# Optimization experiments

Measured on AMD Instinct MI355X. Metric: run time of the kernel, lower is better.

Reference implementation:

```python
import jax, jax.numpy as jnp
import numpy as np

EMBED_DIM = 4096
NQ = 32           # query heads
NKV = 8           # kv heads
HEAD = 128        # head dim
KV_SEQ = 4096
B = 8
T = 32
START_POS = 4064  # end_pos = 4096
SCALE = 1.0 / np.sqrt(HEAD)
THETA = 10000.0


def _rope(x, table_len):
    """Faithful replication of the torch module's RoPE, including its bug:
    the torch code unpacks (B,H,T,D)=x.shape on a (B,T_seq,H,D) tensor, so the
    frequency table (of length table_len) is sliced to the first H (=num heads)
    rows and broadcast along the HEAD axis, not the sequence axis.
    x: (B, T_seq, H, D) float32.
    """
    Bn, Tn, H, D = x.shape
    dh = D // 2
    inv_freq = 1.0 / (THETA ** (jnp.arange(dh, dtype=jnp.float32) / dh))  # (dh,)
    pos = jnp.arange(table_len, dtype=jnp.float32)
    freqs = (pos[:, None] * inv_freq[None, :])[:H]  # (H, dh) -- head-indexed!
    cos = jnp.cos(freqs)[None, None]  # (1,1,H,dh)
    sin = jnp.sin(freqs)[None, None]
    xr, xi = x[..., 0::2], x[..., 1::2]  # complex pairs are consecutive elems
    yr = xr * cos - xi * sin
    yi = xr * sin + xi * cos
    return jnp.stack([yr, yi], axis=-1).reshape(Bn, Tn, H, D)


def setup_inputs() -> dict:
    key = jax.random.key(0)
    ks = jax.random.split(key, 5)
    x = jax.random.normal(ks[0], (B, T, EMBED_DIM), dtype=jnp.float32)
    Wq = jax.random.normal(ks[1], (EMBED_DIM, EMBED_DIM), dtype=jnp.float32) * 0.02
    Wk = jax.random.normal(ks[2], (NKV * HEAD, EMBED_DIM), dtype=jnp.float32) * 0.02
    Wv = jax.random.normal(ks[3], (NKV * HEAD, EMBED_DIM), dtype=jnp.float32) * 0.02
    Wo = jax.random.normal(ks[4], (EMBED_DIM, EMBED_DIM), dtype=jnp.float32) * 0.02
    cache_keys = jnp.zeros((B, KV_SEQ * 2, NKV, HEAD), dtype=jnp.float32)
    cache_values = jnp.zeros((B, KV_SEQ * 2, NKV, HEAD), dtype=jnp.float32)
    return {"x": x, "start_pos": START_POS, "cache_keys": cache_keys,
            "cache_values": cache_values, "Wq": Wq, "Wk": Wk, "Wv": Wv, "Wo": Wo}


def reference(x, start_pos, cache_keys, cache_values, Wq, Wk, Wv, Wo):
    Bn, Tn, C = x.shape
    q = (x @ Wq.T).reshape(Bn, Tn, NQ, HEAD)
    k = (x @ Wk.T).reshape(Bn, Tn, NKV, HEAD)
    v = (x @ Wv.T).reshape(Bn, Tn, NKV, HEAD)
    # rope=True branch: q table built for Tn positions, k table for KV_SEQ
    q = _rope(q, Tn)
    k = _rope(k, KV_SEQ)
    end = start_pos + Tn
    # cache write (torch detaches k/v before writing and reads detached views)
    ck = cache_keys.at[:Bn, start_pos:end].set(jax.lax.stop_gradient(k))
    cv = cache_values.at[:Bn, start_pos:end].set(jax.lax.stop_gradient(v))
    k_full = jax.lax.stop_gradient(ck[:Bn, :end])  # (B, end, NKV, D)
    v_full = jax.lax.stop_gradient(cv[:Bn, :end])
    r = NQ // NKV
    kf = jnp.repeat(k_full.transpose(0, 2, 1, 3), r, axis=1)  # (B, NQ, end, D)
    vf = jnp.repeat(v_full.transpose(0, 2, 1, 3), r, axis=1)
    qh = q.transpose(0, 2, 1, 3)                               # (B, NQ, T, D)
    att = jnp.einsum('bhtd,bhsd->bhts', qh, kf) * SCALE        # (B, NQ, T, end)
    causal = jnp.triu(jnp.ones((end, end), dtype=bool), 1)[-Tn:]  # (T, end)
    att = jnp.where(causal[None, None], -jnp.inf, att)
    att = jax.nn.softmax(att, axis=-1)
    out = jnp.einsum('bhts,bhsd->bhtd', att, vf)
    out = out.transpose(0, 2, 1, 3).reshape(Bn, Tn, C)
    return out @ Wo.T
```

## Files before the change

### kernel.cpp

```cpp
#include <hip/hip_runtime.h>
#include <stdint.h>

#define Bb 8
#define Tt 32
#define Ee 4096
#define NQ 32
#define NKV 8
#define HD 128
#define CACHE_S 8192
#define SSPLIT 8
#define SCALE_F 0.08838834764831845f

typedef _Float16 half8 __attribute__((ext_vector_type(8)));
typedef _Float16 half4 __attribute__((ext_vector_type(4)));
typedef float f32x4 __attribute__((ext_vector_type(4)));

static __device__ __forceinline__ _Float16 f2h(float f) { return (_Float16)f; }

__global__ __launch_bounds__(256) void gemm_nt(
    const float* __restrict__ A, const float* __restrict__ W,
    const float* __restrict__ W2, int n_split,
    float* __restrict__ C, int K, int ldc) {
  __shared__ _Float16 As[64][72];
  __shared__ _Float16 Ws[64][72];
  const int n0 = blockIdx.x * 64;
  const int m0 = blockIdx.y * 64;
  const float* Wp = (n0 < n_split) ? W : W2;
  const int nr0 = (n0 < n_split) ? n0 : (n0 - n_split);
  const int tid = threadIdx.x;
  const int lane = tid & 63;
  const int wave = tid >> 6;
  const int wm = (wave >> 1) * 32;
  const int wn = (wave & 1) * 32;
  const int l15 = lane & 15;
  const int quad = lane >> 4;
  const int sr = tid >> 4;
  const int sc = (tid & 15) * 4;

  f32x4 acc[2][2];
#pragma unroll
  for (int i = 0; i < 2; i++)
#pragma unroll
    for (int j = 0; j < 2; j++) acc[i][j] = f32x4{0.f, 0.f, 0.f, 0.f};

  float4 pa[4], pw[4];
#pragma unroll
  for (int p = 0; p < 4; p++) {
    const int r = sr + p * 16;
    pa[p] = *(const float4*)&A[(size_t)(m0 + r) * K + sc];
    pw[p] = *(const float4*)&Wp[(size_t)(nr0 + r) * K + sc];
  }

  for (int k0 = 0; k0 < K; k0 += 64) {
    __syncthreads();
#pragma unroll
    for (int p = 0; p < 4; p++) {
      const int r = sr + p * 16;
      half4 ha = {f2h(pa[p].x), f2h(pa[p].y), f2h(pa[p].z), f2h(pa[p].w)};
      *(half4*)&As[r][sc] = ha;
      half4 hw = {f2h(pw[p].x), f2h(pw[p].y), f2h(pw[p].z), f2h(pw[p].w)};
      *(half4*)&Ws[r][sc] = hw;
    }
    __syncthreads();
    if (k0 + 64 < K) {
#pragma unroll
      for (int p = 0; p < 4; p++) {
        const int r = sr + p * 16;
        pa[p] = *(const float4*)&A[(size_t)(m0 + r) * K + (k0 + 64 + sc)];
        pw[p] = *(const float4*)&Wp[(size_t)(nr0 + r) * K + (k0 + 64 + sc)];
      }
    }
#pragma unroll
    for (int ks = 0; ks < 2; ks++) {
      const int kc = ks * 32 + quad * 8;
      half8 af[2], wf[2];
#pragma unroll
      for (int i = 0; i < 2; i++) {
        af[i] = *(const half8*)&As[wm + i * 16 + l15][kc];
        wf[i] = *(const half8*)&Ws[wn + i * 16 + l15][kc];
      }
#pragma unroll
      for (int i = 0; i < 2; i++)
#pragma unroll
        for (int j = 0; j < 2; j++)
          acc[i][j] = __builtin_amdgcn_mfma_f32_16x16x32_f16(af[i], wf[j],
                                                             acc[i][j], 0, 0, 0);
    }
  }
#pragma unroll
  for (int i = 0; i < 2; i++) {
    const int mr = m0 + wm + i * 16 + quad * 4;
#pragma unroll
    for (int j = 0; j < 2; j++) {
      const int nc = n0 + wn + j * 16 + l15;
#pragma unroll
      for (int r = 0; r < 4; r++)
        C[(size_t)(mr + r) * ldc + nc] = acc[i][j][r];
    }
  }
}

__global__ __launch_bounds__(256) void rope_scatter(
    const float* __restrict__ qkv, float* __restrict__ qw,
    float* __restrict__ kw, float* __restrict__ vw) {
  const int pid = blockIdx.x * 256 + threadIdx.x;
  const int m = pid / 3072;
  const int c = pid - m * 3072;
  const int n = c * 2;
  const int b = m >> 5;
  const int t = m & 31;
  const float a0 = qkv[(size_t)m * 6144 + n];
  const float a1 = qkv[(size_t)m * 6144 + n + 1];
  if (n < 4096) {
    const int h = n >> 7;
    const int j = (n & 127) >> 1;
    const float invf = powf(10000.0f, -(float)j * (1.0f / 64.0f));
    float sn, cs;
    sincosf((float)h * invf, &sn, &cs);
    float* dst = qw + ((size_t)(b * NQ + h) * Tt + t) * HD + (j << 1);
    dst[0] = a0 * cs - a1 * sn;
    dst[1] = a0 * sn + a1 * cs;
  } else if (n < 5120) {
    const int nn = n - 4096;
    const int h = nn >> 7;
    const int j = (nn & 127) >> 1;
    const float invf = powf(10000.0f, -(float)j * (1.0f / 64.0f));
    float sn, cs;
    sincosf((float)h * invf, &sn, &cs);
    float* dst = kw + ((size_t)(b * NKV + h) * Tt + t) * HD + (j << 1);
    dst[0] = a0 * cs - a1 * sn;
    dst[1] = a0 * sn + a1 * cs;
  } else {
    const int nn = n - 5120;
    const int h = nn >> 7;
    const int d = nn & 127;
    float* dst = vw + ((size_t)(b * NKV + h) * Tt + t) * HD + d;
    dst[0] = a0;
    dst[1] = a1;
  }
}

__global__ __launch_bounds__(256) void attn_partial(
    const float* __restrict__ qw, const float* __restrict__ kw,
    const float* __restrict__ vw, const float* __restrict__ cacheK,
    const float* __restrict__ cacheV, const int* __restrict__ startp,
    float* __restrict__ pO, float* __restrict__ pM, float* __restrict__ pL) {
  const int blk = blockIdx.x;
  const int split = blk & (SSPLIT - 1);
  const int g = (blk / SSPLIT) & (NKV - 1);
  const int b = blk / (SSPLIT * NKV);
  const int start = *startp;
  const int end = start + Tt;
  int cl = ((end + SSPLIT * 32 - 1) / (SSPLIT * 32)) * 32;
  const int s_begin = split * cl;
  int s_end = s_begin + cl;
  if (s_end > end) s_end = end;

  const int tid = threadIdx.x;
  const int lane = tid & 63;
  const int wave = tid >> 6;
  const int l15 = lane & 15;
  const int quad = lane >> 4;
  const int h = g * 4 + wave;

  __shared__ _Float16 Ks[32][136];
  __shared__ _Float16 Vt[128][40];
  __shared__ _Float16 Ps[4][32][40];

  half8 qf[2][4];
#pragma unroll
  for (int mt = 0; mt < 2; mt++) {
    const int t = mt * 16 + l15;
    const float* qrow = qw + ((size_t)(b * NQ + h) * Tt + t) * HD;
#pragma unroll
    for (int ks = 0; ks < 4; ks++) {
      const int d0 = ks * 32 + quad * 8;
      float4 v0 = *(const float4*)&qrow[d0];
      float4 v1 = *(const float4*)&qrow[d0 + 4];
      half8 hq = {f2h(v0.x), f2h(v0.y), f2h(v0.z), f2h(v0.w),
                  f2h(v1.x), f2h(v1.y), f2h(v1.z), f2h(v1.w)};
      qf[mt][ks] = hq;
    }
  }

  f32x4 Oacc[2][8];
#pragma unroll
  for (int mt = 0; mt < 2; mt++)
#pragma unroll
    for (int dt = 0; dt < 8; dt++) Oacc[mt][dt] = f32x4{0.f, 0.f, 0.f, 0.f};
  float mrow[2][4], lrow[2][4];
#pragma unroll
  for (int mt = 0; mt < 2; mt++)
#pragma unroll
    for (int rr = 0; rr < 4; rr++) { mrow[mt][rr] = -1e30f; lrow[mt][rr] = 0.f; }

  const int str = tid >> 3;
  const int stc = (tid & 7) * 4;

  float4 pk[4], pv[4];
  auto load_chunk = [&](int s0) {
    const int sg = s0 + str;
    const bool valid = sg < end;
    const float* krow;
    const float* vrow;
    if (sg < start) {
      const size_t off = (((size_t)b * CACHE_S + sg) * NKV + g) * HD;
      krow = cacheK + off;
      vrow = cacheV + off;
    } else {
      int loc = sg - start;
      if (loc > Tt - 1) loc = Tt - 1;
      const size_t off = ((size_t)(b * NKV + g) * Tt + loc) * HD;
      krow = kw + off;
      vrow = vw + off;
    }
#pragma unroll
    for (int u = 0; u < 4; u++) {
      const int cc = stc + u * 32;
      pk[u] = valid ? *(const float4*)&krow[cc] : make_float4(0.f, 0.f, 0.f, 0.f);
      pv[u] = valid ? *(const float4*)&vrow[cc] : make_float4(0.f, 0.f, 0.f, 0.f);
    }
  };

  load_chunk(s_begin);

  for (int s0 = s_begin; s0 < s_end; s0 += 32) {
    __syncthreads();
#pragma unroll
    for (int u = 0; u < 4; u++) {
      const int cc = stc + u * 32;
      half4 hk = {f2h(pk[u].x), f2h(pk[u].y), f2h(pk[u].z), f2h(pk[u].w)};
      *(half4*)&Ks[str][cc] = hk;
      Vt[cc + 0][str] = f2h(pv[u].x);
      Vt[cc + 1][str] = f2h(pv[u].y);
      Vt[cc + 2][str] = f2h(pv[u].z);
      Vt[cc + 3][str] = f2h(pv[u].w);
    }
    __syncthreads();
    if (s0 + 32 < s_end) load_chunk(s0 + 32);

    f32x4 st[2][2];
#pragma unroll
    for (int mt = 0; mt < 2; mt++)
#pragma unroll
      for (int nt = 0; nt < 2; nt++) st[mt][nt] = f32x4{0.f, 0.f, 0.f, 0.f};
#pragma unroll
    for (int nt = 0; nt < 2; nt++) {
#pragma unroll
      for (int ks = 0; ks < 4; ks++) {
        half8 kf = *(const half8*)&Ks[nt * 16 + l15][ks * 32 + quad * 8];
        st[0][nt] = __builtin_amdgcn_mfma_f32_16x16x32_f16(qf[0][ks], kf, st[0][nt], 0, 0, 0);
        st[1][nt] = __builtin_amdgcn_mfma_f32_16x16x32_f16(qf[1][ks], kf, st[1][nt], 0, 0, 0);
      }
    }
#pragma unroll
    for (int mt = 0; mt < 2; mt++)
#pragma unroll
      for (int nt = 0; nt < 2; nt++)
#pragma unroll
        for (int rr = 0; rr < 4; rr++) {
          const int t = mt * 16 + quad * 4 + rr;
          const int sg = s0 + nt * 16 + l15;
          const float sv = st[mt][nt][rr] * SCALE_F;
          const bool masked = (sg > start + t) || (sg >= end);
          st[mt][nt][rr] = masked ? -1e30f : sv;
        }
#pragma unroll
    for (int mt = 0; mt < 2; mt++) {
      float rmax[4], rsum[4], al[4];
#pragma unroll
      for (int rr = 0; rr < 4; rr++)
        rmax[rr] = fmaxf(st[mt][0][rr], st[mt][1][rr]);
      for (int mm = 1; mm < 16; mm <<= 1)
#pragma unroll
        for (int rr = 0; rr < 4; rr++)
          rmax[rr] = fmaxf(rmax[rr], __shfl_xor(rmax[rr], mm));
#pragma unroll
      for (int rr = 0; rr < 4; rr++) {
        const float mn = fmaxf(mrow[mt][rr], rmax[rr]);
        al[rr] = __expf(mrow[mt][rr] - mn);
        mrow[mt][rr] = mn;
      }
#pragma unroll
      for (int nt = 0; nt < 2; nt++)
#pragma unroll
        for (int rr = 0; rr < 4; rr++)
          st[mt][nt][rr] = __expf(st[mt][nt][rr] - mrow[mt][rr]);
#pragma unroll
      for (int rr = 0; rr < 4; rr++) rsum[rr] = st[mt][0][rr] + st[mt][1][rr];
      for (int mm = 1; mm < 16; mm <<= 1)
#pragma unroll
        for (int rr = 0; rr < 4; rr++) rsum[rr] += __shfl_xor(rsum[rr], mm);
#pragma unroll
      for (int rr = 0; rr < 4; rr++)
        lrow[mt][rr] = lrow[mt][rr] * al[rr] + rsum[rr];
#pragma unroll
      for (int nt = 0; nt < 2; nt++)
#pragma unroll
        for (int rr = 0; rr < 4; rr++)
          Ps[wave][mt * 16 + quad * 4 + rr][nt * 16 + l15] = f2h(st[mt][nt][rr]);
#pragma unroll
      for (int dt = 0; dt < 8; dt++)
#pragma unroll
        for (int rr = 0; rr < 4; rr++) Oacc[mt][dt][rr] *= al[rr];
    }
    half8 pf0 = *(const half8*)&Ps[wave][l15][quad * 8];
    half8 pf1 = *(const half8*)&Ps[wave][16 + l15][quad * 8];
#pragma unroll
    for (int dt = 0; dt < 8; dt++) {
      half8 vf = *(const half8*)&Vt[dt * 16 + l15][quad * 8];
      Oacc[0][dt] = __builtin_amdgcn_mfma_f32_16x16x32_f16(pf0, vf, Oacc[0][dt], 0, 0, 0);
      Oacc[1][dt] = __builtin_amdgcn_mfma_f32_16x16x32_f16(pf1, vf, Oacc[1][dt], 0, 0, 0);
    }
  }

  const size_t rowbase = (size_t)(b * NQ + h) * Tt;
#pragma unroll
  for (int mt = 0; mt < 2; mt++)
#pragma unroll
    for (int rr = 0; rr < 4; rr++) {
      const int t = mt * 16 + quad * 4 + rr;
      const size_t pbase = ((rowbase + t) * SSPLIT + split) * (size_t)HD;
#pragma unroll
      for (int dt = 0; dt < 8; dt++)
        pO[pbase + dt * 16 + l15] = Oacc[mt][dt][rr];
      if (l15 == 0) {
        pM[(rowbase + t) * SSPLIT + split] = mrow[mt][rr];
        pL[(rowbase + t) * SSPLIT + split] = lrow[mt][rr];
      }
    }
}

__global__ __launch_bounds__(128) void attn_combine(
    const float* __restrict__ pO, const float* __restrict__ pM,
    const float* __restrict__ pL, float* __restrict__ att) {
  const int row = blockIdx.x;
  const int d = threadIdx.x;
  float m[SSPLIT], l[SSPLIT];
  float ms = -3.0e30f;
#pragma unroll
  for (int i = 0; i < SSPLIT; i++) {
    m[i] = pM[row * SSPLIT + i];
    l[i] = pL[row * SSPLIT + i];
    ms = fmaxf(ms, m[i]);
  }
  float ls = 0.f, o = 0.f;
#pragma unroll
  for (int i = 0; i < SSPLIT; i++) {
    const float w = __expf(m[i] - ms);
    ls += l[i] * w;
    o += pO[((size_t)row * SSPLIT + i) * HD + d] * w;
  }
  o /= fmaxf(ls, 1e-30f);
  const int b = row / (NQ * Tt);
  const int hh = (row / Tt) % NQ;
  const int t = row % Tt;
  att[((size_t)(b * Tt + t)) * Ee + hh * HD + d] = o;
}

extern "C" void kernel_launch(void* const* d_in, const int* in_sizes, int n_in,
                              void* d_out, int out_size, void* d_ws,
                              size_t ws_size, hipStream_t stream) {
  const float* x = (const float*)d_in[0];
  const int* startp = (const int*)d_in[1];
  const float* cacheK = (const float*)d_in[2];
  const float* cacheV = (const float*)d_in[3];
  const float* Wq = (const float*)d_in[4];
  const float* Wk = (const float*)d_in[5];
  const float* Wv = (const float*)d_in[6];
  const float* Wo = (const float*)d_in[7];
  float* out = (float*)d_out;
  float* ws = (float*)d_ws;

  float* qkv = ws;
  float* pO = ws;
  float* qw = ws + 8388608;
  float* kw = qw + 1048576;
  float* vw = kw + 262144;
  float* pM = vw + 262144;
  float* pL = pM + 65536;
  float* att = pL + 65536;

  const dim3 blk(256);
  gemm_nt<<<dim3(64, 4), blk, 0, stream>>>(x, Wq, Wq, 4096, qkv, 4096, 6144);
  gemm_nt<<<dim3(32, 4), blk, 0, stream>>>(x, Wk, Wv, 1024, qkv + 4096, 4096, 6144);
  rope_scatter<<<dim3(3072), blk, 0, stream>>>(qkv, qw, kw, vw);
  attn_partial<<<dim3(Bb * NKV * SSPLIT), blk, 0, stream>>>(
      qw, kw, vw, cacheK, cacheV, startp, pO, pM, pL);
  attn_combine<<<dim3(Bb * NQ * Tt), dim3(128), 0, stream>>>(pO, pM, pL, att);
  gemm_nt<<<dim3(64, 4), blk, 0, stream>>>(att, Wo, Wo, 4096, out, 4096, 4096);
}
```

Before: 754.6 us.

## Split-K the QKV and output projections and merge the QKV GEMM launches

The separate Q and KV projection GEMMs become one split-K launch over three weight matrices with 4 K-partitions. The partial sums are added inside rope_scatter. The output projection is also split over 2 K-partitions, with a small reduce kernel to sum them. The aim is to fill the GPU's many CUs, since M=256 gave only 256 or 128 blocks before, and to drop one launch. The cost is extra partial-buffer traffic, plus one more kernel for the Wo reduction.

```diff
diff --git a/kernel.cpp b/kernel.cpp
--- a/kernel.cpp
+++ b/kernel.cpp
@@ -17,16 +17,22 @@
 
 static __device__ __forceinline__ _Float16 f2h(float f) { return (_Float16)f; }
 
-__global__ __launch_bounds__(256) void gemm_nt(
-    const float* __restrict__ A, const float* __restrict__ W,
-    const float* __restrict__ W2, int n_split,
-    float* __restrict__ C, int K, int ldc) {
+__global__ __launch_bounds__(256) void gemm_nt_sk(
+    const float* __restrict__ A, const float* __restrict__ W0,
+    const float* __restrict__ W1, const float* __restrict__ W2,
+    int nsplit1, int nsplit2, float* __restrict__ Cpart, size_t part_stride,
+    int K, int Kc, int ldc) {
   __shared__ _Float16 As[64][72];
   __shared__ _Float16 Ws[64][72];
   const int n0 = blockIdx.x * 64;
   const int m0 = blockIdx.y * 64;
-  const float* Wp = (n0 < n_split) ? W : W2;
-  const int nr0 = (n0 < n_split) ? n0 : (n0 - n_split);
+  const int kp = blockIdx.z;
+  const int kbase = kp * Kc;
+  const float* Wp;
+  int nr0;
+  if (n0 < nsplit1) { Wp = W0; nr0 = n0; }
+  else if (n0 < nsplit2) { Wp = W1; nr0 = n0 - nsplit1; }
+  else { Wp = W2; nr0 = n0 - nsplit2; }
   const int tid = threadIdx.x;
   const int lane = tid & 63;
   const int wave = tid >> 6;
@@ -47,11 +53,11 @@
 #pragma unroll
   for (int p = 0; p < 4; p++) {
     const int r = sr + p * 16;
-    pa[p] = *(const float4*)&A[(size_t)(m0 + r) * K + sc];
-    pw[p] = *(const float4*)&Wp[(size_t)(nr0 + r) * K + sc];
-  }
-
-  for (int k0 = 0; k0 < K; k0 += 64) {
+    pa[p] = *(const float4*)&A[(size_t)(m0 + r) * K + kbase + sc];
+    pw[p] = *(const float4*)&Wp[(size_t)(nr0 + r) * K + kbase + sc];
+  }
+
+  for (int k0 = 0; k0 < Kc; k0 += 64) {
     __syncthreads();
 #pragma unroll
     for (int p = 0; p < 4; p++) {
@@ -62,12 +68,12 @@
       *(half4*)&Ws[r][sc] = hw;
     }
     __syncthreads();
-    if (k0 + 64 < K) {
+    if (k0 + 64 < Kc) {
 #pragma unroll
       for (int p = 0; p < 4; p++) {
         const int r = sr + p * 16;
-        pa[p] = *(const float4*)&A[(size_t)(m0 + r) * K + (k0 + 64 + sc)];
-        pw[p] = *(const float4*)&Wp[(size_t)(nr0 + r) * K + (k0 + 64 + sc)];
+        pa[p] = *(const float4*)&A[(size_t)(m0 + r) * K + kbase + k0 + 64 + sc];
+        pw[p] = *(const float4*)&Wp[(size_t)(nr0 + r) * K + kbase + k0 + 64 + sc];
       }
     }
 #pragma unroll
@@ -87,6 +93,7 @@
                                                              acc[i][j], 0, 0, 0);
     }
   }
+  float* Cp = Cpart + (size_t)kp * part_stride;
 #pragma unroll
   for (int i = 0; i < 2; i++) {
     const int mr = m0 + wm + i * 16 + quad * 4;
@@ -95,13 +102,13 @@
       const int nc = n0 + wn + j * 16 + l15;
 #pragma unroll
       for (int r = 0; r < 4; r++)
-        C[(size_t)(mr + r) * ldc + nc] = acc[i][j][r];
+        Cp[(size_t)(mr + r) * ldc + nc] = acc[i][j][r];
     }
   }
 }
 
 __global__ __launch_bounds__(256) void rope_scatter(
-    const float* __restrict__ qkv, float* __restrict__ qw,
+    const float* __restrict__ qkvp, float* __restrict__ qw,
     float* __restrict__ kw, float* __restrict__ vw) {
   const int pid = blockIdx.x * 256 + threadIdx.x;
   const int m = pid / 3072;
@@ -109,8 +116,14 @@
   const int n = c * 2;
   const int b = m >> 5;
   const int t = m & 31;
-  const float a0 = qkv[(size_t)m * 6144 + n];
-  const float a1 = qkv[(size_t)m * 6144 + n + 1];
+  const size_t base = (size_t)m * 6144 + n;
+  float a0 = 0.f, a1 = 0.f;
+#pragma unroll
+  for (int p = 0; p < 4; p++) {
+    const float2 v = *(const float2*)&qkvp[p * 1572864 + base];
+    a0 += v.x;
+    a1 += v.y;
+  }
   if (n < 4096) {
     const int h = n >> 7;
     const int j = (n & 127) >> 1;
@@ -358,6 +371,16 @@
   att[((size_t)(b * Tt + t)) * Ee + hh * HD + d] = o;
 }
 
+__global__ __launch_bounds__(256) void reduce2(const float* __restrict__ p0,
+                                               const float* __restrict__ p1,
+                                               float* __restrict__ out) {
+  const int i = (blockIdx.x * 256 + threadIdx.x) * 4;
+  float4 a = *(const float4*)&p0[i];
+  float4 b = *(const float4*)&p1[i];
+  float4 r = make_float4(a.x + b.x, a.y + b.y, a.z + b.z, a.w + b.w);
+  *(float4*)&out[i] = r;
+}
+
 extern "C" void kernel_launch(void* const* d_in, const int* in_sizes, int n_in,
                               void* d_out, int out_size, void* d_ws,
                               size_t ws_size, hipStream_t stream) {
@@ -372,21 +395,24 @@
   float* out = (float*)d_out;
   float* ws = (float*)d_ws;
 
-  float* qkv = ws;
-  float* pO = ws;
-  float* qw = ws + 8388608;
+  float* qkvp = ws;
+  float* pO = qkvp + 6291456;
+  float* qw = pO + 8388608;
   float* kw = qw + 1048576;
   float* vw = kw + 262144;
   float* pM = vw + 262144;
   float* pL = pM + 65536;
   float* att = pL + 65536;
+  float* woP = att + 1048576;
 
   const dim3 blk(256);
-  gemm_nt<<<dim3(64, 4), blk, 0, stream>>>(x, Wq, Wq, 4096, qkv, 4096, 6144);
-  gemm_nt<<<dim3(32, 4), blk, 0, stream>>>(x, Wk, Wv, 1024, qkv + 4096, 4096, 6144);
-  rope_scatter<<<dim3(3072), blk, 0, stream>>>(qkv, qw, kw, vw);
+  gemm_nt_sk<<<dim3(96, 4, 4), blk, 0, stream>>>(
+      x, Wq, Wk, Wv, 4096, 5120, qkvp, (size_t)256 * 6144, 4096, 1024, 6144);
+  rope_scatter<<<dim3(3072), blk, 0, stream>>>(qkvp, qw, kw, vw);
   attn_partial<<<dim3(Bb * NKV * SSPLIT), blk, 0, stream>>>(
       qw, kw, vw, cacheK, cacheV, startp, pO, pM, pL);
   attn_combine<<<dim3(Bb * NQ * Tt), dim3(128), 0, stream>>>(pO, pM, pL, att);
-  gemm_nt<<<dim3(64, 4), blk, 0, stream>>>(att, Wo, Wo, 4096, out, 4096, 4096);
-}
+  gemm_nt_sk<<<dim3(64, 4, 2), blk, 0, stream>>>(
+      att, Wo, Wo, Wo, 4096, 4096, woP, (size_t)256 * 4096, 4096, 2048, 4096);
+  reduce2<<<dim3(1024), blk, 0, stream>>>(woP, woP + 1048576, out);
+}
```

After: 652.9 us. 1.16x faster.
